# Optimization experiments

Hardware: AMD Instinct MI355X
Metric: run time of the kernel (lower is better)

Reference implementation:

```python
import jax, jax.numpy as jnp
import numpy as np

NEG_SLOPE = 0.2
CONV3_NUM, CONV1_NUM, POLY_NUM = 3, 5, 4
FEAT_DIM = CONV3_NUM * 84 + CONV1_NUM * 12 + POLY_NUM * 12  # 360
DN = ('NCHW', 'OIHW', 'NCHW')


def leaky_relu(x):
    return jnp.where(x >= 0, x, NEG_SLOPE * x)


def conv3x3(x, feat):
    # per-sample dynamic 3x3 conv: feat[:, :81] -> kernel [3,3,3,3], feat[:, 81:84] -> bias
    B = x.shape[0]
    k = feat[:, :81].reshape(B, 3, 3, 3, 3)
    b = feat[:, 81:84]

    def one(xi, ki, bi):
        y = jax.lax.conv_general_dilated(xi[None], ki, (1, 1), 'SAME', dimension_numbers=DN)[0]
        return y + bi[:, None, None]

    return leaky_relu(jax.vmap(one)(x, k, b))


def conv1x1(x, feat):
    B = x.shape[0]
    k = feat[:, :9].reshape(B, 3, 3, 1, 1)
    b = feat[:, 9:12]

    def one(xi, ki, bi):
        y = jax.lax.conv_general_dilated(xi[None], ki, (1, 1), 'VALID', dimension_numbers=DN)[0]
        return y + bi[:, None, None]

    return leaky_relu(jax.vmap(one)(x, k, b))


def conv_stack(x, feature):
    residual = x
    for i in range(CONV3_NUM):
        x = conv3x3(x, feature[:, i * 84:(i + 1) * 84])
    off = CONV3_NUM * 84
    for i in range(CONV1_NUM):
        x = conv1x1(x, feature[:, off + i * 12:off + (i + 1) * 12])
    return residual + x


def att_map(feat, h_mat, w_mat, xc):
    # product over POLY_NUM of (a*h + b*w + c*x + d)
    att = jnp.ones_like(xc)
    for i in range(POLY_NUM):
        a = feat[:, i * 4 + 0].reshape(-1, 1, 1, 1)
        b = feat[:, i * 4 + 1].reshape(-1, 1, 1, 1)
        c = feat[:, i * 4 + 2].reshape(-1, 1, 1, 1)
        d = feat[:, i * 4 + 3].reshape(-1, 1, 1, 1)
        att = att * (a * h_mat + b * w_mat + c * xc + d)
    return att


def apply_attention(x, feature):
    H, W = x.shape[2], x.shape[3]
    h_mat = (jnp.arange(H, dtype=x.dtype) / H).reshape(1, 1, H, 1)
    w_mat = (jnp.arange(W, dtype=x.dtype) / W).reshape(1, 1, 1, W)
    off = CONV3_NUM * 84 + CONV1_NUM * 12
    atts = [att_map(feature[:, off + c * POLY_NUM * 4: off + (c + 1) * POLY_NUM * 4],
                    h_mat, w_mat, x[:, c:c + 1]) for c in range(3)]  # R, G, B
    att = jnp.concatenate(atts, axis=1)
    return x * (1 + att)


def setup_inputs() -> dict:
    key = jax.random.key(0)
    k1, k2, k3 = jax.random.split(key, 3)
    x = jax.random.uniform(k1, (8, 3, 512, 512), dtype=jnp.float32)
    thumb_x = jax.random.uniform(k2, (8, 3, 64, 64), dtype=jnp.float32)
    Wm = jax.random.normal(k3, (3, FEAT_DIM), dtype=jnp.float32) * 0.05
    bm = jnp.zeros((FEAT_DIM,), dtype=jnp.float32)
    return {"x": x, "thumb_x": thumb_x, "Wm": Wm, "bm": bm}


def reference(x, thumb_x, Wm, bm):
    # meta: GAP over thumbnail -> linear -> per-sample hypernetwork features [B, 360]
    feature = jnp.mean(thumb_x, axis=(2, 3)) @ Wm + bm
    x = conv_stack(x, feature)
    x = apply_attention(x, feature)
    thumb = conv_stack(thumb_x, feature)
    thumb = apply_attention(thumb, feature)
    return (x, thumb)
```

## Files before the change

kernel.cpp:

```cpp
#include <hip/hip_runtime.h>


typedef float v2f __attribute__((ext_vector_type(2)));
#define FMA2(a, b, c) __builtin_elementwise_fma((a), (b), (c))

__device__ __forceinline__ v2f leaky2(v2f v) {
    return __builtin_elementwise_max(v, v * 0.2f);
}

__device__ __forceinline__ v2f ldpair(const float* p) {
    v2f r; __builtin_memcpy(&r, p, 8); return r;
}
__device__ __forceinline__ void stpair(float* p, v2f v) {
    __builtin_memcpy(p, &v, 8);
}

constexpr int NCOLS = 73;
constexpr int CSTR  = 23;
constexpr int CHS   = NCOLS * CSTR;
constexpr int BUFSZ = 3 * CHS + 4;

__global__ __launch_bounds__(384) void prep_kernel(
    const float* __restrict__ thumb, const float* __restrict__ Wm,
    const float* __restrict__ bm, float* __restrict__ feat)
{
    const int b = blockIdx.x;
    const int t = threadIdx.x;
    const int ch = t >> 7;
    const int l  = t & 127;
    const float4* p = (const float4*)(thumb + (size_t)b * 3 * 4096);
    float s = 0.f;
#pragma unroll
    for (int k = 0; k < 8; ++k) {
        float4 v = p[ch * 1024 + l + k * 128];
        s += v.x + v.y + v.z + v.w;
    }
    __shared__ float red[384];
    red[t] = s;
    __syncthreads();
    for (int off = 64; off > 0; off >>= 1) {
        if (l < off) red[t] += red[t + off];
        __syncthreads();
    }
    if (t < 360) {
        const float sc = 1.f / 4096.f;
        const float m0 = red[0] * sc, m1 = red[128] * sc, m2 = red[256] * sc;
        feat[b * 360 + t] =
            fmaf(m0, Wm[t], fmaf(m1, Wm[360 + t], fmaf(m2, Wm[720 + t], bm[t])));
    }
}

template<int NC>
__device__ __forceinline__ void conv_rows_pk(
    const float* __restrict__ buf, const float* __restrict__ fw,
    int rb, int gx, v2f acc[3][NC])
{
    const float b0 = fw[81], b1 = fw[82], b2 = fw[83];
#pragma unroll
    for (int c = 0; c < NC; ++c) {
        v2f i0 = {b0, b0}; v2f i1 = {b1, b1}; v2f i2 = {b2, b2};
        acc[0][c] = i0; acc[1][c] = i1; acc[2][c] = i2;
    }
    const int c0 = (gx < 0) ? 3 : gx + 3;
#pragma unroll
    for (int ich = 0; ich < 3; ++ich) {
        const int base = ich * CHS + rb;
        v2f p0[NC + 2], p1[NC + 2], pm[NC + 2];
#pragma unroll
        for (int k = 0; k < NC + 2; ++k) {
            const int cc = (k == 0) ? c0 : (gx + 3 + k);
            p0[k] = ldpair(&buf[base + cc * CSTR]);
            p1[k] = ldpair(&buf[base + cc * CSTR + 2]);
            v2f m = {p0[k].y, p1[k].x};
            pm[k] = m;
        }
#pragma unroll
        for (int dy = 0; dy < 3; ++dy) {
#pragma unroll
            for (int oc = 0; oc < 3; ++oc) {
                const float w0 = fw[oc * 27 + ich * 9 + dy * 3 + 0];
                const float w1 = fw[oc * 27 + ich * 9 + dy * 3 + 1];
                const float w2 = fw[oc * 27 + ich * 9 + dy * 3 + 2];
                v2f W0 = {w0, w0}; v2f W1 = {w1, w1}; v2f W2 = {w2, w2};
#pragma unroll
                for (int c = 0; c < NC; ++c) {
                    const v2f wa = (dy == 0) ? p0[c]     : (dy == 1) ? pm[c]     : p1[c];
                    const v2f wb = (dy == 0) ? p0[c + 1] : (dy == 1) ? pm[c + 1] : p1[c + 1];
                    const v2f wc = (dy == 0) ? p0[c + 2] : (dy == 1) ? pm[c + 2] : p1[c + 2];
                    acc[oc][c] = FMA2(wa, W0, FMA2(wb, W1, FMA2(wc, W2, acc[oc][c])));
                }
            }
        }
    }
}

__global__ __launch_bounds__(256, 4) void conv_att_kernel(
    const float* __restrict__ x, const float* __restrict__ thumb,
    const float* __restrict__ feat, float* __restrict__ out)
{
    __shared__ float buf[BUFSZ];

    int id = blockIdx.x;
    const float* src; float* dst; int H, W, b, trow, tcol;
    if (id < 2048) {
        b = id >> 8; const int t = id & 255;
        H = 512; W = 512; trow = (t >> 3) * 16; tcol = (t & 7) * 64;
        src = x; dst = out;
    } else {
        const int i2 = id - 2048;
        b = i2 >> 2; trow = (i2 & 3) * 16; tcol = 0;
        H = 64; W = 64; src = thumb;
        dst = out + (size_t)8 * 3 * 512 * 512;
    }
    const float* fb = feat + b * 360;
    const int tid = threadIdx.x;

    const float* sbg = src + (size_t)b * 3 * H * W;
    float4 stv[4];
#pragma unroll
    for (int i = 0; i < 4; ++i) {
        const int q = tid + 256 * i;
        const int c = q / 352;
        const int rem = q - c * 352;
        const int mr = rem >> 4;
        const int k  = rem & 15;
        const int gr = trow + mr - 3;
        const int gc0 = tcol + 4 * k;
        float4 v = make_float4(0.f, 0.f, 0.f, 0.f);
        if ((unsigned)gr < (unsigned)H)
            v = *(const float4*)&sbg[(size_t)c * H * W + (size_t)gr * W + gc0];
        stv[i] = v;
    }
    const bool has5 = tid < 32;
    float4 st5 = make_float4(0.f, 0.f, 0.f, 0.f);
    if (has5) {
        const int rem = tid + 1024 - 704;
        const int mr = rem >> 4;
        const int k  = rem & 15;
        const int gr = trow + mr - 3;
        const int gc0 = tcol + 4 * k;
        if ((unsigned)gr < (unsigned)H)
            st5 = *(const float4*)&sbg[(size_t)2 * H * W + (size_t)gr * W + gc0];
    }
    const bool hasH = tid < 132;
    float4 hv = make_float4(0.f, 0.f, 0.f, 0.f);
    int hc = 0, hmr = 0, hside = 0;
    if (hasH) {
        hc = tid / 44;
        const int rem = tid - hc * 44;
        hmr = rem >> 1;
        hside = rem & 1;
        const int gr = trow + hmr - 3;
        const int gc0 = tcol + (hside ? 64 : -4);
        const bool rok = (unsigned)gr < (unsigned)H;
        const float* gp = sbg + (size_t)hc * H * W + (size_t)(rok ? gr : 0) * W;
        if (rok && (unsigned)gc0 <= (unsigned)(W - 4)) {
            hv = *(const float4*)&gp[gc0];
        } else {
            hv.x = (rok && (unsigned)(gc0 + 0) < (unsigned)W) ? gp[gc0 + 0] : 0.f;
            hv.y = (rok && (unsigned)(gc0 + 1) < (unsigned)W) ? gp[gc0 + 1] : 0.f;
            hv.z = (rok && (unsigned)(gc0 + 2) < (unsigned)W) ? gp[gc0 + 2] : 0.f;
            hv.w = (rok && (unsigned)(gc0 + 3) < (unsigned)W) ? gp[gc0 + 3] : 0.f;
        }
    }
#pragma unroll
    for (int i = 0; i < 4; ++i) {
        const int q = tid + 256 * i;
        const int c = q / 352;
        const int rem = q - c * 352;
        const int mr = rem >> 4;
        const int k  = rem & 15;
        float* bp = &buf[c * CHS + (4 * k + 4) * CSTR + mr];
        bp[0] = stv[i].x; bp[CSTR] = stv[i].y;
        bp[2 * CSTR] = stv[i].z; bp[3 * CSTR] = stv[i].w;
    }
    if (has5) {
        const int rem = tid + 1024 - 704;
        const int mr = rem >> 4;
        const int k  = rem & 15;
        float* bp = &buf[2 * CHS + (4 * k + 4) * CSTR + mr];
        bp[0] = st5.x; bp[CSTR] = st5.y; bp[2 * CSTR] = st5.z; bp[3 * CSTR] = st5.w;
    }
    if (hasH) {
        float* bp = &buf[hc * CHS + (hside ? 68 : 0) * CSTR + hmr];
        bp[0] = hv.x; bp[CSTR] = hv.y; bp[2 * CSTR] = hv.z; bp[3 * CSTR] = hv.w;
    }
    if (tid < 66) {
        const int c = tid / 22, mr = tid - c * 22;
        buf[c * CHS + 72 * CSTR + mr] = 0.f;
    }
    __syncthreads();

    const bool act1 = tid < 180;
    int s1, gx1;
    if (tid < 160) { s1 = tid >> 4; gx1 = 4 * (tid & 15); }
    else { const int v = tid - 160; s1 = v >> 1; gx1 = (v & 1) ? 64 : -4; }
    v2f acc[3][4];
    if (act1) conv_rows_pk<4>(buf, fb, 2 * s1, gx1, acc);

    const int s3e = tid >> 5;
    const int gx3e = 2 * (tid & 31);
    v2f res2[3][2];
#pragma unroll
    for (int ch = 0; ch < 3; ++ch)
#pragma unroll
        for (int c = 0; c < 2; ++c)
            res2[ch][c] = ldpair(&buf[ch * CHS + (gx3e + 4 + c) * CSTR + (2 * s3e + 3)]);
    __syncthreads();

    if (act1) {
#pragma unroll
        for (int oc = 0; oc < 3; ++oc)
#pragma unroll
            for (int c = 0; c < 4; ++c)
                stpair(&buf[oc * CHS + (gx1 + 4 + c) * CSTR + (2 * s1 + 1)],
                       leaky2(acc[oc][c]));
    }
    __syncthreads();

    const bool act2 = tid < 162;
    int s2, gx2;
    if (tid < 144) { s2 = tid >> 4; gx2 = 4 * (tid & 15); }
    else { const int v = tid - 144; s2 = v >> 1; gx2 = (v & 1) ? 64 : -4; }
    if (act2) conv_rows_pk<4>(buf, fb + 84, 2 * s2 + 1, gx2, acc);
    __syncthreads();

    if (act2) {
#pragma unroll
        for (int oc = 0; oc < 3; ++oc)
#pragma unroll
            for (int c = 0; c < 4; ++c)
                stpair(&buf[oc * CHS + (gx2 + 4 + c) * CSTR + (2 * s2 + 2)],
                       leaky2(acc[oc][c]));
    }
    __syncthreads();

    {
        v2f y[3][2];
        {
            v2f acc3[3][2];
            conv_rows_pk<2>(buf, fb + 168, 2 * s3e + 2, gx3e, acc3);
#pragma unroll
            for (int oc = 0; oc < 3; ++oc)
#pragma unroll
                for (int c = 0; c < 2; ++c) y[oc][c] = leaky2(acc3[oc][c]);
        }

#pragma unroll
        for (int lay = 0; lay < 5; ++lay) {
            const float* fw = fb + 252 + lay * 12;
            v2f W0 = {fw[0], fw[0]}; v2f W1 = {fw[1], fw[1]}; v2f W2 = {fw[2], fw[2]};
            v2f W3 = {fw[3], fw[3]}; v2f W4 = {fw[4], fw[4]}; v2f W5 = {fw[5], fw[5]};
            v2f W6 = {fw[6], fw[6]}; v2f W7 = {fw[7], fw[7]}; v2f W8 = {fw[8], fw[8]};
            v2f C0 = {fw[9], fw[9]}; v2f C1 = {fw[10], fw[10]}; v2f C2 = {fw[11], fw[11]};
            v2f z0[2], z1[2], z2[2];
#pragma unroll
            for (int c = 0; c < 2; ++c) {
                z0[c] = FMA2(y[0][c], W0, FMA2(y[1][c], W1, FMA2(y[2][c], W2, C0)));
                z1[c] = FMA2(y[0][c], W3, FMA2(y[1][c], W4, FMA2(y[2][c], W5, C1)));
                z2[c] = FMA2(y[0][c], W6, FMA2(y[1][c], W7, FMA2(y[2][c], W8, C2)));
            }
#pragma unroll
            for (int c = 0; c < 2; ++c) {
                y[0][c] = leaky2(z0[c]);
                y[1][c] = leaky2(z1[c]);
                y[2][c] = leaky2(z2[c]);
            }
        }

        const float invH = 1.f / (float)H;
        const float invW = 1.f / (float)W;
        const int gr0 = trow + 2 * s3e;
        v2f h2 = {(float)gr0 * invH, (float)(gr0 + 1) * invH};
        const float wb = (float)(tcol + gx3e) * invW;
        const v2f one = {1.f, 1.f};
#pragma unroll
        for (int ch = 0; ch < 3; ++ch) {
            const float* fp = fb + 312 + ch * 16;
            v2f PA0 = {fp[0], fp[0]},  PB0 = {fp[1], fp[1]},  PC0 = {fp[2], fp[2]},  PD0 = {fp[3], fp[3]};
            v2f PA1 = {fp[4], fp[4]},  PB1 = {fp[5], fp[5]},  PC1 = {fp[6], fp[6]},  PD1 = {fp[7], fp[7]};
            v2f PA2 = {fp[8], fp[8]},  PB2 = {fp[9], fp[9]},  PC2 = {fp[10], fp[10]}, PD2 = {fp[11], fp[11]};
            v2f PA3 = {fp[12], fp[12]}, PB3 = {fp[13], fp[13]}, PC3 = {fp[14], fp[14]}, PD3 = {fp[15], fp[15]};
            v2f t0 = FMA2(PA0, h2, PD0);
            v2f t1 = FMA2(PA1, h2, PD1);
            v2f t2 = FMA2(PA2, h2, PD2);
            v2f t3 = FMA2(PA3, h2, PD3);
            v2f o[2];
#pragma unroll
            for (int c = 0; c < 2; ++c) {
                const float wcs = wb + (float)c * invW;
                v2f Wc = {wcs, wcs};
                v2f v = y[ch][c] + res2[ch][c];
                v2f a = FMA2(PB0, Wc, FMA2(PC0, v, t0));
                a = a * FMA2(PB1, Wc, FMA2(PC1, v, t1));
                a = a * FMA2(PB2, Wc, FMA2(PC2, v, t2));
                a = a * FMA2(PB3, Wc, FMA2(PC3, v, t3));
                o[c] = v * (one + a);
            }
            v2f ra = {o[0].x, o[1].x};
            v2f rb2 = {o[0].y, o[1].y};
            float* dp = &dst[((size_t)(b * 3 + ch) * H + gr0) * W + tcol + gx3e];
            __builtin_memcpy(dp, &ra, 8);
            __builtin_memcpy(dp + W, &rb2, 8);
        }
    }
}

extern "C" void kernel_launch(void* const* d_in, const int* in_sizes, int n_in,
                              void* d_out, int out_size, void* d_ws, size_t ws_size,
                              hipStream_t stream) {
    const float* x = (const float*)d_in[0];
    const float* thumb = (const float*)d_in[1];
    const float* Wm = (const float*)d_in[2];
    const float* bm = (const float*)d_in[3];
    float* out = (float*)d_out;
    float* feat = (float*)d_ws;

    prep_kernel<<<8, 384, 0, stream>>>(thumb, Wm, bm, feat);
    conv_att_kernel<<<2080, 256, 0, stream>>>(x, thumb, feat, out);
}
```

Measured before the change: 107.0 us.

## Widen conv tiles to 128 columns to cut halo recompute and block count

Doubles the tile width of the fused conv+attention kernel from 64 to 128 columns. Each thread now computes 8 column pairs per conv layer and handles two output positions in the final stage. The thumbnail tiles (64 wide) are masked by bounds checks. This halves the grid and reduces the redundant halo loads and recompute, but uses more shared memory and registers, so launch bounds drop to 3 blocks per SM. A lower occupancy is the risk.

```diff
diff --git a/kernel.cpp b/kernel.cpp
--- a/kernel.cpp
+++ b/kernel.cpp
@@ -15,7 +15,7 @@
     __builtin_memcpy(p, &v, 8);
 }
 
-constexpr int NCOLS = 73;
+constexpr int NCOLS = 137;
 constexpr int CSTR  = 23;
 constexpr int CHS   = NCOLS * CSTR;
 constexpr int BUFSZ = 3 * CHS + 4;
@@ -94,7 +94,7 @@
     }
 }
 
-__global__ __launch_bounds__(256, 4) void conv_att_kernel(
+__global__ __launch_bounds__(256, 3) void conv_att_kernel(
     const float* __restrict__ x, const float* __restrict__ thumb,
     const float* __restrict__ feat, float* __restrict__ out)
 {
@@ -102,12 +102,12 @@
 
     int id = blockIdx.x;
     const float* src; float* dst; int H, W, b, trow, tcol;
-    if (id < 2048) {
-        b = id >> 8; const int t = id & 255;
-        H = 512; W = 512; trow = (t >> 3) * 16; tcol = (t & 7) * 64;
+    if (id < 1024) {
+        b = id >> 7; const int t = id & 127;
+        H = 512; W = 512; trow = (t >> 2) * 16; tcol = (t & 3) * 128;
         src = x; dst = out;
     } else {
-        const int i2 = id - 2048;
+        const int i2 = id - 1024;
         b = i2 >> 2; trow = (i2 & 3) * 16; tcol = 0;
         H = 64; W = 64; src = thumb;
         dst = out + (size_t)8 * 3 * 512 * 512;
@@ -116,31 +116,31 @@
     const int tid = threadIdx.x;
 
     const float* sbg = src + (size_t)b * 3 * H * W;
-    float4 stv[4];
-#pragma unroll
-    for (int i = 0; i < 4; ++i) {
+    float4 stv[8];
+#pragma unroll
+    for (int i = 0; i < 8; ++i) {
         const int q = tid + 256 * i;
-        const int c = q / 352;
-        const int rem = q - c * 352;
-        const int mr = rem >> 4;
-        const int k  = rem & 15;
+        const int c = q / 704;
+        const int rem = q - c * 704;
+        const int mr = rem >> 5;
+        const int k  = rem & 31;
         const int gr = trow + mr - 3;
         const int gc0 = tcol + 4 * k;
         float4 v = make_float4(0.f, 0.f, 0.f, 0.f);
-        if ((unsigned)gr < (unsigned)H)
+        if ((unsigned)gr < (unsigned)H && (unsigned)gc0 <= (unsigned)(W - 4))
             v = *(const float4*)&sbg[(size_t)c * H * W + (size_t)gr * W + gc0];
         stv[i] = v;
     }
-    const bool has5 = tid < 32;
-    float4 st5 = make_float4(0.f, 0.f, 0.f, 0.f);
-    if (has5) {
-        const int rem = tid + 1024 - 704;
-        const int mr = rem >> 4;
-        const int k  = rem & 15;
+    const bool has9 = tid < 64;
+    float4 st9 = make_float4(0.f, 0.f, 0.f, 0.f);
+    if (has9) {
+        const int rem = 640 + tid;
+        const int mr = rem >> 5;
+        const int k  = rem & 31;
         const int gr = trow + mr - 3;
         const int gc0 = tcol + 4 * k;
-        if ((unsigned)gr < (unsigned)H)
-            st5 = *(const float4*)&sbg[(size_t)2 * H * W + (size_t)gr * W + gc0];
+        if ((unsigned)gr < (unsigned)H && (unsigned)gc0 <= (unsigned)(W - 4))
+            st9 = *(const float4*)&sbg[(size_t)2 * H * W + (size_t)gr * W + gc0];
     }
     const bool hasH = tid < 132;
     float4 hv = make_float4(0.f, 0.f, 0.f, 0.f);
@@ -151,7 +151,7 @@
         hmr = rem >> 1;
         hside = rem & 1;
         const int gr = trow + hmr - 3;
-        const int gc0 = tcol + (hside ? 64 : -4);
+        const int gc0 = tcol + (hside ? 128 : -4);
         const bool rok = (unsigned)gr < (unsigned)H;
         const float* gp = sbg + (size_t)hc * H * W + (size_t)(rok ? gr : 0) * W;
         if (rok && (unsigned)gc0 <= (unsigned)(W - 4)) {
@@ -164,78 +164,86 @@
         }
     }
 #pragma unroll
-    for (int i = 0; i < 4; ++i) {
+    for (int i = 0; i < 8; ++i) {
         const int q = tid + 256 * i;
-        const int c = q / 352;
-        const int rem = q - c * 352;
-        const int mr = rem >> 4;
-        const int k  = rem & 15;
+        const int c = q / 704;
+        const int rem = q - c * 704;
+        const int mr = rem >> 5;
+        const int k  = rem & 31;
         float* bp = &buf[c * CHS + (4 * k + 4) * CSTR + mr];
         bp[0] = stv[i].x; bp[CSTR] = stv[i].y;
         bp[2 * CSTR] = stv[i].z; bp[3 * CSTR] = stv[i].w;
     }
-    if (has5) {
-        const int rem = tid + 1024 - 704;
-        const int mr = rem >> 4;
-        const int k  = rem & 15;
+    if (has9) {
+        const int rem = 640 + tid;
+        const int mr = rem >> 5;
+        const int k  = rem & 31;
         float* bp = &buf[2 * CHS + (4 * k + 4) * CSTR + mr];
-        bp[0] = st5.x; bp[CSTR] = st5.y; bp[2 * CSTR] = st5.z; bp[3 * CSTR] = st5.w;
+        bp[0] = st9.x; bp[CSTR] = st9.y; bp[2 * CSTR] = st9.z; bp[3 * CSTR] = st9.w;
     }
     if (hasH) {
-        float* bp = &buf[hc * CHS + (hside ? 68 : 0) * CSTR + hmr];
+        float* bp = &buf[hc * CHS + (hside ? 132 : 0) * CSTR + hmr];
         bp[0] = hv.x; bp[CSTR] = hv.y; bp[2 * CSTR] = hv.z; bp[3 * CSTR] = hv.w;
     }
     if (tid < 66) {
         const int c = tid / 22, mr = tid - c * 22;
-        buf[c * CHS + 72 * CSTR + mr] = 0.f;
-    }
-    __syncthreads();
-
-    const bool act1 = tid < 180;
-    int s1, gx1;
-    if (tid < 160) { s1 = tid >> 4; gx1 = 4 * (tid & 15); }
-    else { const int v = tid - 160; s1 = v >> 1; gx1 = (v & 1) ? 64 : -4; }
-    v2f acc[3][4];
-    if (act1) conv_rows_pk<4>(buf, fb, 2 * s1, gx1, acc);
-
-    const int s3e = tid >> 5;
-    const int gx3e = 2 * (tid & 31);
-    v2f res2[3][2];
-#pragma unroll
-    for (int ch = 0; ch < 3; ++ch)
-#pragma unroll
-        for (int c = 0; c < 2; ++c)
-            res2[ch][c] = ldpair(&buf[ch * CHS + (gx3e + 4 + c) * CSTR + (2 * s3e + 3)]);
+        buf[c * CHS + 136 * CSTR + mr] = 0.f;
+    }
+    __syncthreads();
+
+    const bool act1 = tid < 170;
+    int s1 = 0, gx1 = 0;
+    if (act1) { s1 = tid / 17; gx1 = 8 * (tid - s1 * 17) - 4; }
+    v2f acc[3][8];
+    if (act1) conv_rows_pk<8>(buf, fb, 2 * s1, gx1, acc);
+
+    v2f res2[2][3][2];
+#pragma unroll
+    for (int r = 0; r < 2; ++r) {
+        const int u = tid + 256 * r;
+        const int s3e = u >> 6;
+        const int gx3e = 2 * (u & 63);
+#pragma unroll
+        for (int ch = 0; ch < 3; ++ch)
+#pragma unroll
+            for (int c = 0; c < 2; ++c)
+                res2[r][ch][c] = ldpair(&buf[ch * CHS + (gx3e + 4 + c) * CSTR + (2 * s3e + 3)]);
+    }
     __syncthreads();
 
     if (act1) {
 #pragma unroll
         for (int oc = 0; oc < 3; ++oc)
 #pragma unroll
-            for (int c = 0; c < 4; ++c)
+            for (int c = 0; c < 8; ++c)
                 stpair(&buf[oc * CHS + (gx1 + 4 + c) * CSTR + (2 * s1 + 1)],
                        leaky2(acc[oc][c]));
     }
     __syncthreads();
 
-    const bool act2 = tid < 162;
-    int s2, gx2;
-    if (tid < 144) { s2 = tid >> 4; gx2 = 4 * (tid & 15); }
-    else { const int v = tid - 144; s2 = v >> 1; gx2 = (v & 1) ? 64 : -4; }
-    if (act2) conv_rows_pk<4>(buf, fb + 84, 2 * s2 + 1, gx2, acc);
+    const bool act2 = tid < 153;
+    int s2 = 0, gx2 = 0;
+    if (act2) { s2 = tid / 17; gx2 = 8 * (tid - s2 * 17) - 4; }
+    if (act2) conv_rows_pk<8>(buf, fb + 84, 2 * s2 + 1, gx2, acc);
     __syncthreads();
 
     if (act2) {
 #pragma unroll
         for (int oc = 0; oc < 3; ++oc)
 #pragma unroll
-            for (int c = 0; c < 4; ++c)
+            for (int c = 0; c < 8; ++c)
                 stpair(&buf[oc * CHS + (gx2 + 4 + c) * CSTR + (2 * s2 + 2)],
                        leaky2(acc[oc][c]));
     }
     __syncthreads();
 
-    {
+    const float invH = 1.f / (float)H;
+    const float invW = 1.f / (float)W;
+#pragma unroll
+    for (int r = 0; r < 2; ++r) {
+        const int u = tid + 256 * r;
+        const int s3e = u >> 6;
+        const int gx3e = 2 * (u & 63);
         v2f y[3][2];
         {
             v2f acc3[3][2];
@@ -268,40 +276,41 @@
             }
         }
 
-        const float invH = 1.f / (float)H;
-        const float invW = 1.f / (float)W;
         const int gr0 = trow + 2 * s3e;
-        v2f h2 = {(float)gr0 * invH, (float)(gr0 + 1) * invH};
-        const float wb = (float)(tcol + gx3e) * invW;
-        const v2f one = {1.f, 1.f};
-#pragma unroll
-        for (int ch = 0; ch < 3; ++ch) {
-            const float* fp = fb + 312 + ch * 16;
-            v2f PA0 = {fp[0], fp[0]},  PB0 = {fp[1], fp[1]},  PC0 = {fp[2], fp[2]},  PD0 = {fp[3], fp[3]};
-            v2f PA1 = {fp[4], fp[4]},  PB1 = {fp[5], fp[5]},  PC1 = {fp[6], fp[6]},  PD1 = {fp[7], fp[7]};
-            v2f PA2 = {fp[8], fp[8]},  PB2 = {fp[9], fp[9]},  PC2 = {fp[10], fp[10]}, PD2 = {fp[11], fp[11]};
-            v2f PA3 = {fp[12], fp[12]}, PB3 = {fp[13], fp[13]}, PC3 = {fp[14], fp[14]}, PD3 = {fp[15], fp[15]};
-            v2f t0 = FMA2(PA0, h2, PD0);
-            v2f t1 = FMA2(PA1, h2, PD1);
-            v2f t2 = FMA2(PA2, h2, PD2);
-            v2f t3 = FMA2(PA3, h2, PD3);
-            v2f o[2];
-#pragma unroll
-            for (int c = 0; c < 2; ++c) {
-                const float wcs = wb + (float)c * invW;
-                v2f Wc = {wcs, wcs};
-                v2f v = y[ch][c] + res2[ch][c];
-                v2f a = FMA2(PB0, Wc, FMA2(PC0, v, t0));
-                a = a * FMA2(PB1, Wc, FMA2(PC1, v, t1));
-                a = a * FMA2(PB2, Wc, FMA2(PC2, v, t2));
-                a = a * FMA2(PB3, Wc, FMA2(PC3, v, t3));
-                o[c] = v * (one + a);
+        const bool stok = (tcol + gx3e) <= (W - 2);
+        if (stok) {
+            v2f h2 = {(float)gr0 * invH, (float)(gr0 + 1) * invH};
+            const float wb = (float)(tcol + gx3e) * invW;
+            const v2f one = {1.f, 1.f};
+#pragma unroll
+            for (int ch = 0; ch < 3; ++ch) {
+                const float* fp = fb + 312 + ch * 16;
+                v2f PA0 = {fp[0], fp[0]},  PB0 = {fp[1], fp[1]},  PC0 = {fp[2], fp[2]},  PD0 = {fp[3], fp[3]};
+                v2f PA1 = {fp[4], fp[4]},  PB1 = {fp[5], fp[5]},  PC1 = {fp[6], fp[6]},  PD1 = {fp[7], fp[7]};
+                v2f PA2 = {fp[8], fp[8]},  PB2 = {fp[9], fp[9]},  PC2 = {fp[10], fp[10]}, PD2 = {fp[11], fp[11]};
+                v2f PA3 = {fp[12], fp[12]}, PB3 = {fp[13], fp[13]}, PC3 = {fp[14], fp[14]}, PD3 = {fp[15], fp[15]};
+                v2f t0 = FMA2(PA0, h2, PD0);
+                v2f t1 = FMA2(PA1, h2, PD1);
+                v2f t2 = FMA2(PA2, h2, PD2);
+                v2f t3 = FMA2(PA3, h2, PD3);
+                v2f o[2];
+#pragma unroll
+                for (int c = 0; c < 2; ++c) {
+                    const float wcs = wb + (float)c * invW;
+                    v2f Wc = {wcs, wcs};
+                    v2f v = y[ch][c] + res2[r][ch][c];
+                    v2f a = FMA2(PB0, Wc, FMA2(PC0, v, t0));
+                    a = a * FMA2(PB1, Wc, FMA2(PC1, v, t1));
+                    a = a * FMA2(PB2, Wc, FMA2(PC2, v, t2));
+                    a = a * FMA2(PB3, Wc, FMA2(PC3, v, t3));
+                    o[c] = v * (one + a);
+                }
+                v2f ra = {o[0].x, o[1].x};
+                v2f rb2 = {o[0].y, o[1].y};
+                float* dp = &dst[((size_t)(b * 3 + ch) * H + gr0) * W + tcol + gx3e];
+                __builtin_memcpy(dp, &ra, 8);
+                __builtin_memcpy(dp + W, &rb2, 8);
             }
-            v2f ra = {o[0].x, o[1].x};
-            v2f rb2 = {o[0].y, o[1].y};
-            float* dp = &dst[((size_t)(b * 3 + ch) * H + gr0) * W + tcol + gx3e];
-            __builtin_memcpy(dp, &ra, 8);
-            __builtin_memcpy(dp + W, &rb2, 8);
         }
     }
 }
@@ -317,5 +326,5 @@
     float* feat = (float*)d_ws;
 
     prep_kernel<<<8, 384, 0, stream>>>(thumb, Wm, bm, feat);
-    conv_att_kernel<<<2080, 256, 0, stream>>>(x, thumb, feat, out);
-}
+    conv_att_kernel<<<1056, 256, 0, stream>>>(x, thumb, feat, out);
+}
```

Result: slower. 122.3 us (+14.3%).

## Process two tiles per block, prefetching the second tile into registers

Applied to the files above, without the earlier changes.

Each block now handles two adjacent tiles. Both tiles' global loads are issued up front into registers, so the second tile's memory latency is hidden behind the first tile's conv compute. The grid is halved and shared memory is doubled to two buffers. This adds register pressure from holding two staging sets, and the larger LDS footprint may lower occupancy under the (256,4) launch bounds.

```diff
diff --git a/kernel.cpp b/kernel.cpp
--- a/kernel.cpp
+++ b/kernel.cpp
@@ -94,29 +94,12 @@
     }
 }
 
-__global__ __launch_bounds__(256, 4) void conv_att_kernel(
-    const float* __restrict__ x, const float* __restrict__ thumb,
-    const float* __restrict__ feat, float* __restrict__ out)
-{
-    __shared__ float buf[BUFSZ];
-
-    int id = blockIdx.x;
-    const float* src; float* dst; int H, W, b, trow, tcol;
-    if (id < 2048) {
-        b = id >> 8; const int t = id & 255;
-        H = 512; W = 512; trow = (t >> 3) * 16; tcol = (t & 7) * 64;
-        src = x; dst = out;
-    } else {
-        const int i2 = id - 2048;
-        b = i2 >> 2; trow = (i2 & 3) * 16; tcol = 0;
-        H = 64; W = 64; src = thumb;
-        dst = out + (size_t)8 * 3 * 512 * 512;
-    }
-    const float* fb = feat + b * 360;
-    const int tid = threadIdx.x;
-
-    const float* sbg = src + (size_t)b * 3 * H * W;
-    float4 stv[4];
+struct StageRegs { float4 stv[4]; float4 st5; float4 hv; };
+
+__device__ __forceinline__ void stage_load(
+    const float* __restrict__ sbg, int H, int W, int trow, int tcol, int tid,
+    StageRegs& R)
+{
 #pragma unroll
     for (int i = 0; i < 4; ++i) {
         const int q = tid + 256 * i;
@@ -129,31 +112,29 @@
         float4 v = make_float4(0.f, 0.f, 0.f, 0.f);
         if ((unsigned)gr < (unsigned)H)
             v = *(const float4*)&sbg[(size_t)c * H * W + (size_t)gr * W + gc0];
-        stv[i] = v;
-    }
-    const bool has5 = tid < 32;
-    float4 st5 = make_float4(0.f, 0.f, 0.f, 0.f);
-    if (has5) {
+        R.stv[i] = v;
+    }
+    R.st5 = make_float4(0.f, 0.f, 0.f, 0.f);
+    if (tid < 32) {
         const int rem = tid + 1024 - 704;
         const int mr = rem >> 4;
         const int k  = rem & 15;
         const int gr = trow + mr - 3;
         const int gc0 = tcol + 4 * k;
         if ((unsigned)gr < (unsigned)H)
-            st5 = *(const float4*)&sbg[(size_t)2 * H * W + (size_t)gr * W + gc0];
-    }
-    const bool hasH = tid < 132;
-    float4 hv = make_float4(0.f, 0.f, 0.f, 0.f);
-    int hc = 0, hmr = 0, hside = 0;
-    if (hasH) {
-        hc = tid / 44;
+            R.st5 = *(const float4*)&sbg[(size_t)2 * H * W + (size_t)gr * W + gc0];
+    }
+    R.hv = make_float4(0.f, 0.f, 0.f, 0.f);
+    if (tid < 132) {
+        const int hc = tid / 44;
         const int rem = tid - hc * 44;
-        hmr = rem >> 1;
-        hside = rem & 1;
+        const int hmr = rem >> 1;
+        const int hside = rem & 1;
         const int gr = trow + hmr - 3;
         const int gc0 = tcol + (hside ? 64 : -4);
         const bool rok = (unsigned)gr < (unsigned)H;
         const float* gp = sbg + (size_t)hc * H * W + (size_t)(rok ? gr : 0) * W;
+        float4 hv = make_float4(0.f, 0.f, 0.f, 0.f);
         if (rok && (unsigned)gc0 <= (unsigned)(W - 4)) {
             hv = *(const float4*)&gp[gc0];
         } else {
@@ -162,7 +143,13 @@
             hv.z = (rok && (unsigned)(gc0 + 2) < (unsigned)W) ? gp[gc0 + 2] : 0.f;
             hv.w = (rok && (unsigned)(gc0 + 3) < (unsigned)W) ? gp[gc0 + 3] : 0.f;
         }
-    }
+        R.hv = hv;
+    }
+}
+
+__device__ __forceinline__ void stage_write(
+    float* __restrict__ buf, int tid, const StageRegs& R)
+{
 #pragma unroll
     for (int i = 0; i < 4; ++i) {
         const int q = tid + 256 * i;
@@ -171,137 +158,188 @@
         const int mr = rem >> 4;
         const int k  = rem & 15;
         float* bp = &buf[c * CHS + (4 * k + 4) * CSTR + mr];
-        bp[0] = stv[i].x; bp[CSTR] = stv[i].y;
-        bp[2 * CSTR] = stv[i].z; bp[3 * CSTR] = stv[i].w;
-    }
-    if (has5) {
+        bp[0] = R.stv[i].x; bp[CSTR] = R.stv[i].y;
+        bp[2 * CSTR] = R.stv[i].z; bp[3 * CSTR] = R.stv[i].w;
+    }
+    if (tid < 32) {
         const int rem = tid + 1024 - 704;
         const int mr = rem >> 4;
         const int k  = rem & 15;
         float* bp = &buf[2 * CHS + (4 * k + 4) * CSTR + mr];
-        bp[0] = st5.x; bp[CSTR] = st5.y; bp[2 * CSTR] = st5.z; bp[3 * CSTR] = st5.w;
-    }
-    if (hasH) {
+        bp[0] = R.st5.x; bp[CSTR] = R.st5.y; bp[2 * CSTR] = R.st5.z; bp[3 * CSTR] = R.st5.w;
+    }
+    if (tid < 132) {
+        const int hc = tid / 44;
+        const int rem = tid - hc * 44;
+        const int hmr = rem >> 1;
+        const int hside = rem & 1;
         float* bp = &buf[hc * CHS + (hside ? 68 : 0) * CSTR + hmr];
-        bp[0] = hv.x; bp[CSTR] = hv.y; bp[2 * CSTR] = hv.z; bp[3 * CSTR] = hv.w;
-    }
+        bp[0] = R.hv.x; bp[CSTR] = R.hv.y; bp[2 * CSTR] = R.hv.z; bp[3 * CSTR] = R.hv.w;
+    }
+}
+
+__global__ __launch_bounds__(256, 4) void conv_att_kernel(
+    const float* __restrict__ x, const float* __restrict__ thumb,
+    const float* __restrict__ feat, float* __restrict__ out)
+{
+    __shared__ float buf2[2][BUFSZ];
+
+    const int id = blockIdx.x;
+    const float* src; float* dst; int H, W, b;
+    int trow0, tcol0, trow1, tcol1;
+    if (id < 1024) {
+        b = id >> 7; const int t = id & 127;
+        const int band = t >> 2, pr = t & 3;
+        H = 512; W = 512;
+        trow0 = band * 16; tcol0 = pr * 128;
+        trow1 = band * 16; tcol1 = pr * 128 + 64;
+        src = x; dst = out;
+    } else {
+        const int i2 = id - 1024;
+        b = i2 >> 1; const int p = i2 & 1;
+        H = 64; W = 64;
+        trow0 = p * 32; tcol0 = 0;
+        trow1 = p * 32 + 16; tcol1 = 0;
+        src = thumb;
+        dst = out + (size_t)8 * 3 * 512 * 512;
+    }
+    const float* fb = feat + b * 360;
+    const int tid = threadIdx.x;
+    const float* sbg = src + (size_t)b * 3 * H * W;
+
+    StageRegs R0, R1;
+    stage_load(sbg, H, W, trow0, tcol0, tid, R0);
+    stage_load(sbg, H, W, trow1, tcol1, tid, R1);
+    stage_write(&buf2[0][0], tid, R0);
     if (tid < 66) {
         const int c = tid / 22, mr = tid - c * 22;
-        buf[c * CHS + 72 * CSTR + mr] = 0.f;
+        buf2[0][c * CHS + 72 * CSTR + mr] = 0.f;
+        buf2[1][c * CHS + 72 * CSTR + mr] = 0.f;
     }
     __syncthreads();
 
-    const bool act1 = tid < 180;
-    int s1, gx1;
-    if (tid < 160) { s1 = tid >> 4; gx1 = 4 * (tid & 15); }
-    else { const int v = tid - 160; s1 = v >> 1; gx1 = (v & 1) ? 64 : -4; }
-    v2f acc[3][4];
-    if (act1) conv_rows_pk<4>(buf, fb, 2 * s1, gx1, acc);
-
-    const int s3e = tid >> 5;
-    const int gx3e = 2 * (tid & 31);
-    v2f res2[3][2];
-#pragma unroll
-    for (int ch = 0; ch < 3; ++ch)
-#pragma unroll
-        for (int c = 0; c < 2; ++c)
-            res2[ch][c] = ldpair(&buf[ch * CHS + (gx3e + 4 + c) * CSTR + (2 * s3e + 3)]);
-    __syncthreads();
-
-    if (act1) {
-#pragma unroll
-        for (int oc = 0; oc < 3; ++oc)
-#pragma unroll
-            for (int c = 0; c < 4; ++c)
-                stpair(&buf[oc * CHS + (gx1 + 4 + c) * CSTR + (2 * s1 + 1)],
-                       leaky2(acc[oc][c]));
-    }
-    __syncthreads();
-
-    const bool act2 = tid < 162;
-    int s2, gx2;
-    if (tid < 144) { s2 = tid >> 4; gx2 = 4 * (tid & 15); }
-    else { const int v = tid - 144; s2 = v >> 1; gx2 = (v & 1) ? 64 : -4; }
-    if (act2) conv_rows_pk<4>(buf, fb + 84, 2 * s2 + 1, gx2, acc);
-    __syncthreads();
-
-    if (act2) {
-#pragma unroll
-        for (int oc = 0; oc < 3; ++oc)
-#pragma unroll
-            for (int c = 0; c < 4; ++c)
-                stpair(&buf[oc * CHS + (gx2 + 4 + c) * CSTR + (2 * s2 + 2)],
-                       leaky2(acc[oc][c]));
-    }
-    __syncthreads();
-
-    {
-        v2f y[3][2];
+#pragma unroll
+    for (int ti = 0; ti < 2; ++ti) {
+        float* buf = &buf2[ti][0];
+        const int trow = ti ? trow1 : trow0;
+        const int tcol = ti ? tcol1 : tcol0;
+        if (ti == 1) {
+            stage_write(buf, tid, R1);
+            __syncthreads();
+        }
+
+        const bool act1 = tid < 180;
+        int s1, gx1;
+        if (tid < 160) { s1 = tid >> 4; gx1 = 4 * (tid & 15); }
+        else { const int v = tid - 160; s1 = v >> 1; gx1 = (v & 1) ? 64 : -4; }
+        v2f acc[3][4];
+        if (act1) conv_rows_pk<4>(buf, fb, 2 * s1, gx1, acc);
+
+        const int s3e = tid >> 5;
+        const int gx3e = 2 * (tid & 31);
+        v2f res2[3][2];
+#pragma unroll
+        for (int ch = 0; ch < 3; ++ch)
+#pragma unroll
+            for (int c = 0; c < 2; ++c)
+                res2[ch][c] = ldpair(&buf[ch * CHS + (gx3e + 4 + c) * CSTR + (2 * s3e + 3)]);
+        __syncthreads();
+
+        if (act1) {
+#pragma unroll
+            for (int oc = 0; oc < 3; ++oc)
+#pragma unroll
+                for (int c = 0; c < 4; ++c)
+                    stpair(&buf[oc * CHS + (gx1 + 4 + c) * CSTR + (2 * s1 + 1)],
+                           leaky2(acc[oc][c]));
+        }
+        __syncthreads();
+
+        const bool act2 = tid < 162;
+        int s2, gx2;
+        if (tid < 144) { s2 = tid >> 4; gx2 = 4 * (tid & 15); }
+        else { const int v = tid - 144; s2 = v >> 1; gx2 = (v & 1) ? 64 : -4; }
+        if (act2) conv_rows_pk<4>(buf, fb + 84, 2 * s2 + 1, gx2, acc);
+        __syncthreads();
+
+        if (act2) {
+#pragma unroll
+            for (int oc = 0; oc < 3; ++oc)
+#pragma unroll
+                for (int c = 0; c < 4; ++c)
+                    stpair(&buf[oc * CHS + (gx2 + 4 + c) * CSTR + (2 * s2 + 2)],
+                           leaky2(acc[oc][c]));
+        }
+        __syncthreads();
+
         {
-            v2f acc3[3][2];
-            conv_rows_pk<2>(buf, fb + 168, 2 * s3e + 2, gx3e, acc3);
-#pragma unroll
-            for (int oc = 0; oc < 3; ++oc)
-#pragma unroll
-                for (int c = 0; c < 2; ++c) y[oc][c] = leaky2(acc3[oc][c]);
-        }
-
-#pragma unroll
-        for (int lay = 0; lay < 5; ++lay) {
-            const float* fw = fb + 252 + lay * 12;
-            v2f W0 = {fw[0], fw[0]}; v2f W1 = {fw[1], fw[1]}; v2f W2 = {fw[2], fw[2]};
-            v2f W3 = {fw[3], fw[3]}; v2f W4 = {fw[4], fw[4]}; v2f W5 = {fw[5], fw[5]};
-            v2f W6 = {fw[6], fw[6]}; v2f W7 = {fw[7], fw[7]}; v2f W8 = {fw[8], fw[8]};
-            v2f C0 = {fw[9], fw[9]}; v2f C1 = {fw[10], fw[10]}; v2f C2 = {fw[11], fw[11]};
-            v2f z0[2], z1[2], z2[2];
-#pragma unroll
-            for (int c = 0; c < 2; ++c) {
-                z0[c] = FMA2(y[0][c], W0, FMA2(y[1][c], W1, FMA2(y[2][c], W2, C0)));
-                z1[c] = FMA2(y[0][c], W3, FMA2(y[1][c], W4, FMA2(y[2][c], W5, C1)));
-                z2[c] = FMA2(y[0][c], W6, FMA2(y[1][c], W7, FMA2(y[2][c], W8, C2)));
+            v2f y[3][2];
+            {
+                v2f acc3[3][2];
+                conv_rows_pk<2>(buf, fb + 168, 2 * s3e + 2, gx3e, acc3);
+#pragma unroll
+                for (int oc = 0; oc < 3; ++oc)
+#pragma unroll
+                    for (int c = 0; c < 2; ++c) y[oc][c] = leaky2(acc3[oc][c]);
             }
-#pragma unroll
-            for (int c = 0; c < 2; ++c) {
-                y[0][c] = leaky2(z0[c]);
-                y[1][c] = leaky2(z1[c]);
-                y[2][c] = leaky2(z2[c]);
+
+#pragma unroll
+            for (int lay = 0; lay < 5; ++lay) {
+                const float* fw = fb + 252 + lay * 12;
+                v2f W0 = {fw[0], fw[0]}; v2f W1 = {fw[1], fw[1]}; v2f W2 = {fw[2], fw[2]};
+                v2f W3 = {fw[3], fw[3]}; v2f W4 = {fw[4], fw[4]}; v2f W5 = {fw[5], fw[5]};
+                v2f W6 = {fw[6], fw[6]}; v2f W7 = {fw[7], fw[7]}; v2f W8 = {fw[8], fw[8]};
+                v2f C0 = {fw[9], fw[9]}; v2f C1 = {fw[10], fw[10]}; v2f C2 = {fw[11], fw[11]};
+                v2f z0[2], z1[2], z2[2];
+#pragma unroll
+                for (int c = 0; c < 2; ++c) {
+                    z0[c] = FMA2(y[0][c], W0, FMA2(y[1][c], W1, FMA2(y[2][c], W2, C0)));
+                    z1[c] = FMA2(y[0][c], W3, FMA2(y[1][c], W4, FMA2(y[2][c], W5, C1)));
+                    z2[c] = FMA2(y[0][c], W6, FMA2(y[1][c], W7, FMA2(y[2][c], W8, C2)));
+                }
+#pragma unroll
+                for (int c = 0; c < 2; ++c) {
+                    y[0][c] = leaky2(z0[c]);
+                    y[1][c] = leaky2(z1[c]);
+                    y[2][c] = leaky2(z2[c]);
+                }
             }
-        }
-
-        const float invH = 1.f / (float)H;
-        const float invW = 1.f / (float)W;
-        const int gr0 = trow + 2 * s3e;
-        v2f h2 = {(float)gr0 * invH, (float)(gr0 + 1) * invH};
-        const float wb = (float)(tcol + gx3e) * invW;
-        const v2f one = {1.f, 1.f};
-#pragma unroll
-        for (int ch = 0; ch < 3; ++ch) {
-            const float* fp = fb + 312 + ch * 16;
-            v2f PA0 = {fp[0], fp[0]},  PB0 = {fp[1], fp[1]},  PC0 = {fp[2], fp[2]},  PD0 = {fp[3], fp[3]};
-            v2f PA1 = {fp[4], fp[4]},  PB1 = {fp[5], fp[5]},  PC1 = {fp[6], fp[6]},  PD1 = {fp[7], fp[7]};
-            v2f PA2 = {fp[8], fp[8]},  PB2 = {fp[9], fp[9]},  PC2 = {fp[10], fp[10]}, PD2 = {fp[11], fp[11]};
-            v2f PA3 = {fp[12], fp[12]}, PB3 = {fp[13], fp[13]}, PC3 = {fp[14], fp[14]}, PD3 = {fp[15], fp[15]};
-            v2f t0 = FMA2(PA0, h2, PD0);
-            v2f t1 = FMA2(PA1, h2, PD1);
-            v2f t2 = FMA2(PA2, h2, PD2);
-            v2f t3 = FMA2(PA3, h2, PD3);
-            v2f o[2];
-#pragma unroll
-            for (int c = 0; c < 2; ++c) {
-                const float wcs = wb + (float)c * invW;
-                v2f Wc = {wcs, wcs};
-                v2f v = y[ch][c] + res2[ch][c];
-                v2f a = FMA2(PB0, Wc, FMA2(PC0, v, t0));
-                a = a * FMA2(PB1, Wc, FMA2(PC1, v, t1));
-                a = a * FMA2(PB2, Wc, FMA2(PC2, v, t2));
-                a = a * FMA2(PB3, Wc, FMA2(PC3, v, t3));
-                o[c] = v * (one + a);
+
+            const float invH = 1.f / (float)H;
+            const float invW = 1.f / (float)W;
+            const int gr0 = trow + 2 * s3e;
+            v2f h2 = {(float)gr0 * invH, (float)(gr0 + 1) * invH};
+            const float wb = (float)(tcol + gx3e) * invW;
+            const v2f one = {1.f, 1.f};
+#pragma unroll
+            for (int ch = 0; ch < 3; ++ch) {
+                const float* fp = fb + 312 + ch * 16;
+                v2f PA0 = {fp[0], fp[0]},  PB0 = {fp[1], fp[1]},  PC0 = {fp[2], fp[2]},  PD0 = {fp[3], fp[3]};
+                v2f PA1 = {fp[4], fp[4]},  PB1 = {fp[5], fp[5]},  PC1 = {fp[6], fp[6]},  PD1 = {fp[7], fp[7]};
+                v2f PA2 = {fp[8], fp[8]},  PB2 = {fp[9], fp[9]},  PC2 = {fp[10], fp[10]}, PD2 = {fp[11], fp[11]};
+                v2f PA3 = {fp[12], fp[12]}, PB3 = {fp[13], fp[13]}, PC3 = {fp[14], fp[14]}, PD3 = {fp[15], fp[15]};
+                v2f t0 = FMA2(PA0, h2, PD0);
+                v2f t1 = FMA2(PA1, h2, PD1);
+                v2f t2 = FMA2(PA2, h2, PD2);
+                v2f t3 = FMA2(PA3, h2, PD3);
+                v2f o[2];
+#pragma unroll
+                for (int c = 0; c < 2; ++c) {
+                    const float wcs = wb + (float)c * invW;
+                    v2f Wc = {wcs, wcs};
+                    v2f v = y[ch][c] + res2[ch][c];
+                    v2f a = FMA2(PB0, Wc, FMA2(PC0, v, t0));
+                    a = a * FMA2(PB1, Wc, FMA2(PC1, v, t1));
+                    a = a * FMA2(PB2, Wc, FMA2(PC2, v, t2));
+                    a = a * FMA2(PB3, Wc, FMA2(PC3, v, t3));
+                    o[c] = v * (one + a);
+                }
+                v2f ra = {o[0].x, o[1].x};
+                v2f rb2 = {o[0].y, o[1].y};
+                float* dp = &dst[((size_t)(b * 3 + ch) * H + gr0) * W + tcol + gx3e];
+                __builtin_memcpy(dp, &ra, 8);
+                __builtin_memcpy(dp + W, &rb2, 8);
             }
-            v2f ra = {o[0].x, o[1].x};
-            v2f rb2 = {o[0].y, o[1].y};
-            float* dp = &dst[((size_t)(b * 3 + ch) * H + gr0) * W + tcol + gx3e];
-            __builtin_memcpy(dp, &ra, 8);
-            __builtin_memcpy(dp + W, &rb2, 8);
         }
     }
 }
@@ -317,5 +355,5 @@
     float* feat = (float*)d_ws;
 
     prep_kernel<<<8, 384, 0, stream>>>(thumb, Wm, bm, feat);
-    conv_att_kernel<<<2080, 256, 0, stream>>>(x, thumb, feat, out);
-}
+    conv_att_kernel<<<1040, 256, 0, stream>>>(x, thumb, feat, out);
+}
```

Result: slower. 114.7 us (+7.3%).
